# Kernel tuning notes

Hardware: AMD Instinct MI355X
Metric: run time of the kernel (lower is better)

Reference implementation:

```python
import jax, jax.numpy as jnp
import numpy as np

N_NODES = 100000
N_EDGES = 1600000
HIDDEN = 64
IN_CH = 6  # 3 (direction) + 3 (node feature part)
BN_EPS = 1e-5


def setup_inputs() -> dict:
    key = jax.random.key(0)
    ks = jax.random.split(key, 16)
    inp = {
        "x": jax.random.normal(ks[0], (N_NODES, 3), dtype=jnp.float32),
        "pos": jax.random.normal(ks[1], (N_NODES, 3), dtype=jnp.float32),
        "edge_index": jax.random.randint(ks[2], (2, N_EDGES), 0, N_NODES, dtype=jnp.int64),
    }
    dims = [IN_CH, HIDDEN, HIDDEN, HIDDEN]
    for i in range(3):
        din, dout = dims[i], dims[i + 1]
        inp[f"W{i+1}"] = jax.random.normal(ks[3 + 4 * i], (din, dout), dtype=jnp.float32) * (1.0 / np.sqrt(din))
        inp[f"b{i+1}"] = jnp.zeros((dout,), dtype=jnp.float32)
        inp[f"g{i+1}"] = jnp.ones((dout,), dtype=jnp.float32)   # BN gamma
        inp[f"be{i+1}"] = jnp.zeros((dout,), dtype=jnp.float32)  # BN beta
    return inp


def _mlp_layer(h, W, b, g, be):
    # Linear -> ReLU -> BatchNorm1d (training mode, biased variance like torch)
    h = jax.nn.relu(h @ W + b)
    mu = jnp.mean(h, axis=0)
    var = jnp.mean((h - mu) ** 2, axis=0)
    return g * (h - mu) * jax.lax.rsqrt(var + BN_EPS) + be


def reference(x, pos, edge_index, W1, b1, g1, be1, W2, b2, g2, be2, W3, b3, g3, be3):
    n = x.shape[0]
    xp = jnp.concatenate([pos, x], axis=1)             # [N, 3+F]
    src, dst = edge_index[0], edge_index[1]            # j = src, i = dst (PyG source_to_target)
    x_j = xp[src]                                      # [E, 3+F]
    x_i = xp[dst]
    direction = x_j[:, :3] - x_i[:, :3]                # [E, 3]
    # NOTE: source uses torch.norm with no dim => single global scalar norm
    direction = direction / jnp.linalg.norm(direction)
    h = jnp.concatenate([direction, x_i[:, 3:]], axis=-1)  # [E, IN_CH]
    h = _mlp_layer(h, W1, b1, g1, be1)
    h = _mlp_layer(h, W2, b2, g2, be2)
    h = _mlp_layer(h, W3, b3, g3, be3)                 # [E, HIDDEN]
    out = jax.ops.segment_max(h, dst, num_segments=n)  # scatter-max aggregation
    out = jnp.where(jnp.isfinite(out), out, 0.0)       # PyG fills empty segments with 0
    return out
```

## Files before the change

### kernel.cpp

```cpp
#include <hip/hip_runtime.h>
#include <stdint.h>

typedef unsigned short u16;
typedef unsigned int u32;
typedef __attribute__((ext_vector_type(8))) short short8;
typedef __attribute__((ext_vector_type(4))) float floatx4;

#define BN_EPS 1e-5f
#define NPB 256
#define NBMAX 512

__device__ __forceinline__ float bf2f(u16 u) { return __uint_as_float(((unsigned)u) << 16); }
__device__ __forceinline__ u16 f2bf(float f) {
  unsigned u = __float_as_uint(f);
  u += 0x7FFFu + ((u >> 16) & 1u);
  return (u16)(u >> 16);
}

__global__ void k_init(float* __restrict__ stats, u32* __restrict__ bucketTotal) {
  for (int i = threadIdx.x; i < 1024; i += blockDim.x) stats[i] = 0.f;
  for (int i = threadIdx.x; i < NBMAX + 1; i += blockDim.x) bucketTotal[i] = 0u;
}

__global__ void k_norm_hist(const int* __restrict__ ei, const float* __restrict__ pos,
                            int E, int NB, float* __restrict__ stats,
                            u32* __restrict__ bucketTotal) {
  __shared__ u32 lh[NBMAX];
  __shared__ float red[16];
  for (int i = threadIdx.x; i < NB; i += blockDim.x) lh[i] = 0u;
  __syncthreads();
  int tid = blockIdx.x * blockDim.x + threadIdx.x;
  int stride = gridDim.x * blockDim.x;
  float acc = 0.f;
  for (int e = tid; e < E; e += stride) {
    int s = ei[e], d = ei[E + e];
    float d0 = pos[3 * s + 0] - pos[3 * d + 0];
    float d1 = pos[3 * s + 1] - pos[3 * d + 1];
    float d2 = pos[3 * s + 2] - pos[3 * d + 2];
    acc = fmaf(d0, d0, acc);
    acc = fmaf(d1, d1, acc);
    acc = fmaf(d2, d2, acc);
    atomicAdd(&lh[d >> 8], 1u);
  }
#pragma unroll
  for (int off = 32; off > 0; off >>= 1) acc += __shfl_down(acc, off, 64);
  if ((threadIdx.x & 63) == 0) red[threadIdx.x >> 6] = acc;
  __syncthreads();
  if (threadIdx.x == 0) {
    float s = 0.f;
    for (int w = 0; w < (int)(blockDim.x >> 6); w++) s += red[w];
    atomicAdd(&stats[0], s);
  }
  for (int i = threadIdx.x; i < NB; i += blockDim.x)
    if (lh[i]) atomicAdd(&bucketTotal[i], lh[i]);
}

__global__ void k_scan(const u32* __restrict__ bucketTotal, u32* __restrict__ base,
                       u32* __restrict__ cursor, int NB) {
  if (threadIdx.x == 0 && blockIdx.x == 0) {
    u32 run = 0;
    for (int b = 0; b < NB; b++) {
      base[b] = run;
      cursor[b] = run;
      run += bucketTotal[b];
    }
    base[NB] = run;
  }
}

__global__ void k_place(const int* __restrict__ ei, int E, int NB,
                        u32* __restrict__ cursor, u32* __restrict__ sorted) {
  __shared__ u32 lh[NBMAX];
  __shared__ u32 lbase[NBMAX];
  for (int i = threadIdx.x; i < NB; i += blockDim.x) lh[i] = 0u;
  __syncthreads();
  int tid = blockIdx.x * blockDim.x + threadIdx.x;
  int stride = gridDim.x * blockDim.x;
  for (int e = tid; e < E; e += stride) atomicAdd(&lh[ei[E + e] >> 8], 1u);
  __syncthreads();
  for (int i = threadIdx.x; i < NB; i += blockDim.x) {
    u32 c = lh[i];
    lbase[i] = c ? atomicAdd(&cursor[i], c) : 0u;
    lh[i] = 0u;
  }
  __syncthreads();
  for (int e = tid; e < E; e += stride) {
    int d = ei[E + e];
    int b = d >> 8;
    u32 slot = lbase[b] + atomicAdd(&lh[b], 1u);
    sorted[slot] = ((u32)e << 8) | (u32)(d & 255);
  }
}

__global__ __launch_bounds__(256) void k_bucket_sort(
    const u32* __restrict__ sp, const u32* __restrict__ bbase,
    u32* __restrict__ sorted2, u32* __restrict__ nodeBase) {
  __shared__ u32 hist[NPB];
  __shared__ u32 sbase[NPB];
  int b = blockIdx.x;
  u32 start = bbase[b];
  int cnt = (int)(bbase[b + 1] - start);
  int t = threadIdx.x;
  hist[t] = 0u;
  __syncthreads();
  for (int i = t; i < cnt; i += 256) atomicAdd(&hist[sp[start + i] & 255u], 1u);
  __syncthreads();
  u32 hv = hist[t];
  sbase[t] = hv;
  __syncthreads();
  for (int off = 1; off < 256; off <<= 1) {
    u32 xx = (t >= off) ? sbase[t - off] : 0u;
    __syncthreads();
    sbase[t] += xx;
    __syncthreads();
  }
  u32 excl = sbase[t] - hv;
  __syncthreads();
  sbase[t] = start + excl;
  nodeBase[b * NPB + t] = start + excl;
  hist[t] = 0u;
  __syncthreads();
  for (int i = t; i < cnt; i += 256) {
    u32 pk = sp[start + i];
    u32 ln = pk & 255u;
    u32 slot = sbase[ln] + atomicAdd(&hist[ln], 1u);
    sorted2[slot] = pk >> 8;
  }
}

__global__ __launch_bounds__(256) void k_node_max(
    const u32* __restrict__ sorted2, const u32* __restrict__ nodeBase,
    const u16* __restrict__ h, const float* __restrict__ sc3,
    const float* __restrict__ sh3, float* __restrict__ outf, int N) {
  int lane = threadIdx.x & 63;
  int w = ((int)blockIdx.x * (blockDim.x >> 6)) + (threadIdx.x >> 6);
  int nw = (int)gridDim.x * (blockDim.x >> 6);
  float sc = sc3[lane], sh = sh3[lane];
  for (int n = w; n < N; n += nw) {
    u32 s0 = nodeBase[n];
    int cnt = (int)(nodeBase[n + 1] - s0);
    float v = -3.4e38f;
    for (int i0 = 0; i0 < cnt; i0 += 64) {
      int lim = cnt - i0;
      if (lim > 64) lim = 64;
      u32 myid = (lane < lim) ? sorted2[s0 + i0 + lane] : 0u;
#pragma unroll 4
      for (int i = 0; i < lim; i++) {
        u32 e = __shfl(myid, i, 64);
        float hf = bf2f(h[(long)e * 64 + lane]);
        v = fmaxf(v, fmaf(hf, sc, sh));
      }
    }
    outf[(long)n * 64 + lane] = (cnt == 0) ? 0.f : v;
  }
}

__global__ __launch_bounds__(256) void k_layer1(
    const int* __restrict__ ei, const float* __restrict__ pos,
    const float* __restrict__ x, const float* __restrict__ W1,
    const float* __restrict__ b1, u16* __restrict__ h,
    const float* __restrict__ stats, float* __restrict__ gsum,
    float* __restrict__ gsq, int E) {
  __shared__ float in6[6][256];
  __shared__ float ssum[64], ssq[64];
  float invn = 1.0f / sqrtf(stats[0]);
  int t = threadIdx.x;
  int lane = t & 63;
  int wv = t >> 6;
  float w[6];
#pragma unroll
  for (int k = 0; k < 6; k++) w[k] = W1[k * 64 + lane];
  float bias = b1[lane];
  float psum = 0.f, psq = 0.f;

  int chunks = (E + 255) >> 8;
  for (int c = blockIdx.x; c < chunks; c += gridDim.x) {
    long e0 = (long)c << 8;
    int e = (int)e0 + t;
    float v[6] = {0.f, 0.f, 0.f, 0.f, 0.f, 0.f};
    if (e < E) {
      int s = ei[e], d = ei[E + e];
      float p0 = pos[3 * s + 0], p1 = pos[3 * s + 1], p2 = pos[3 * s + 2];
      float q0 = pos[3 * d + 0], q1 = pos[3 * d + 1], q2 = pos[3 * d + 2];
      v[0] = (p0 - q0) * invn;
      v[1] = (p1 - q1) * invn;
      v[2] = (p2 - q2) * invn;
      v[3] = x[3 * d + 0];
      v[4] = x[3 * d + 1];
      v[5] = x[3 * d + 2];
    }
    __syncthreads();
#pragma unroll
    for (int k = 0; k < 6; k++) in6[k][t] = v[k];
    __syncthreads();
    int lim = E - (int)e0;
    if (lim > 256) lim = 256;
    int base = wv * 64;
#pragma unroll 4
    for (int i = 0; i < 64; i++) {
      int el = base + i;
      if (el >= lim) break;
      float acc = bias;
#pragma unroll
      for (int k = 0; k < 6; k++) acc = fmaf(in6[k][el], w[k], acc);
      acc = fmaxf(acc, 0.f);
      u16 hb = f2bf(acc);
      h[(e0 + el) * 64 + lane] = hb;
      float hf = bf2f(hb);
      psum += hf;
      psq = fmaf(hf, hf, psq);
    }
  }
  if (t < 64) { ssum[t] = 0.f; ssq[t] = 0.f; }
  __syncthreads();
  atomicAdd(&ssum[lane], psum);
  atomicAdd(&ssq[lane], psq);
  __syncthreads();
  if (t < 64) {
    atomicAdd(&gsum[t], ssum[t]);
    atomicAdd(&gsq[t], ssq[t]);
  }
}

__global__ void k_fin(const float* __restrict__ gsum, const float* __restrict__ gsq,
                      const float* __restrict__ g, const float* __restrict__ be,
                      float* __restrict__ scale, float* __restrict__ shift, float invE) {
  int c = threadIdx.x;
  float mu = gsum[c] * invE;
  float var = gsq[c] * invE - mu * mu;
  float s = g[c] * rsqrtf(var + BN_EPS);
  scale[c] = s;
  shift[c] = be[c] - mu * s;
}

__global__ __launch_bounds__(256) void k_layer_mfma(
    u16* h, const float* __restrict__ W, const float* __restrict__ b,
    const float* __restrict__ scale_in, const float* __restrict__ shift_in,
    float* __restrict__ gsum, float* __restrict__ gsq, int E) {
  int lane = threadIdx.x & 63;
  int m = lane & 15;
  int q = lane >> 4;

  short8 bf[4][2];
  float bias[4];
#pragma unroll
  for (int t = 0; t < 4; t++) {
    int n = t * 16 + m;
    float bb = b[n];
    for (int k = 0; k < 64; k++) bb = fmaf(shift_in[k], W[k * 64 + n], bb);
    bias[t] = bb;
#pragma unroll
    for (int s = 0; s < 2; s++)
#pragma unroll
      for (int j = 0; j < 8; j++) {
        int k = s * 32 + q * 8 + j;
        bf[t][s][j] = (short)f2bf(W[k * 64 + n] * scale_in[k]);
      }
  }

  float psum[4] = {0.f, 0.f, 0.f, 0.f}, psq[4] = {0.f, 0.f, 0.f, 0.f};

  int tiles = E >> 4;
  int gw = ((int)blockIdx.x * (blockDim.x >> 6)) + (threadIdx.x >> 6);
  int nw = (int)gridDim.x * (blockDim.x >> 6);

  for (int tile = gw; tile < tiles; tile += nw) {
    long e0 = (long)tile * 16;
    const u16* rowp = h + (e0 + m) * 64 + q * 8;
    short8 a0 = *(const short8*)(rowp);
    short8 a1 = *(const short8*)(rowp + 32);
    floatx4 acc[4];
#pragma unroll
    for (int t = 0; t < 4; t++) acc[t] = (floatx4){0.f, 0.f, 0.f, 0.f};
#pragma unroll
    for (int t = 0; t < 4; t++)
      acc[t] = __builtin_amdgcn_mfma_f32_16x16x32_bf16(a0, bf[t][0], acc[t], 0, 0, 0);
#pragma unroll
    for (int t = 0; t < 4; t++)
      acc[t] = __builtin_amdgcn_mfma_f32_16x16x32_bf16(a1, bf[t][1], acc[t], 0, 0, 0);

#pragma unroll
    for (int t = 0; t < 4; t++) {
#pragma unroll
      for (int r = 0; r < 4; r++) {
        float v = acc[t][r] + bias[t];
        v = fmaxf(v, 0.f);
        u16 hb = f2bf(v);
        h[(e0 + q * 4 + r) * 64 + t * 16 + m] = hb;
        float hf = bf2f(hb);
        psum[t] += hf;
        psq[t] = fmaf(hf, hf, psq[t]);
      }
    }
  }

#pragma unroll
  for (int t = 0; t < 4; t++) {
    psum[t] += __shfl_xor(psum[t], 16, 64);
    psum[t] += __shfl_xor(psum[t], 32, 64);
    psq[t] += __shfl_xor(psq[t], 16, 64);
    psq[t] += __shfl_xor(psq[t], 32, 64);
  }
  __shared__ float ssum[64], ssq[64];
  if (threadIdx.x < 64) { ssum[threadIdx.x] = 0.f; ssq[threadIdx.x] = 0.f; }
  __syncthreads();
  if (q == 0) {
#pragma unroll
    for (int t = 0; t < 4; t++) {
      atomicAdd(&ssum[t * 16 + m], psum[t]);
      atomicAdd(&ssq[t * 16 + m], psq[t]);
    }
  }
  __syncthreads();
  if (threadIdx.x < 64) {
    atomicAdd(&gsum[threadIdx.x], ssum[threadIdx.x]);
    atomicAdd(&gsq[threadIdx.x], ssq[threadIdx.x]);
  }
}

__global__ void k_initout(float* __restrict__ outf, long n, float* __restrict__ stats,
                          u32* __restrict__ bucketTotal) {
  long i = (long)blockIdx.x * blockDim.x + threadIdx.x;
  long stride = (long)gridDim.x * blockDim.x;
  for (long j = i; j < n; j += stride) outf[j] = __uint_as_float(0xFF800000u);
  if (i < 1024) stats[i] = 0.f;
  if (i < NBMAX + 1) bucketTotal[i] = 0u;
}
__global__ void k_scatter(const int* __restrict__ ei, const u16* __restrict__ h,
                          const float* __restrict__ scale, const float* __restrict__ shift,
                          float* outf, int E) {
  int lane = threadIdx.x & 63;
  int gw = ((int)blockIdx.x * (blockDim.x >> 6)) + (threadIdx.x >> 6);
  int nw = (int)gridDim.x * (blockDim.x >> 6);
  float sc = scale[lane], sh = shift[lane];
  for (int e = gw; e < E; e += nw) {
    int d = ei[E + e];
    float v = fmaf(bf2f(h[(long)e * 64 + lane]), sc, sh);
    float* addr = outf + (long)d * 64 + lane;
    if (v >= 0.f)
      atomicMax((int*)addr, __float_as_int(v));
    else
      atomicMin((unsigned int*)addr, __float_as_uint(v));
  }
}
__global__ void k_out(float* __restrict__ outf, long n) {
  long i = (long)blockIdx.x * blockDim.x + threadIdx.x;
  long stride = (long)gridDim.x * blockDim.x;
  for (long j = i; j < n; j += stride) {
    float v = outf[j];
    unsigned u = __float_as_uint(v);
    if ((u & 0x7F800000u) == 0x7F800000u) v = 0.f;
    outf[j] = v;
  }
}

extern "C" void kernel_launch(void* const* d_in, const int* in_sizes, int n_in,
                              void* d_out, int out_size, void* d_ws, size_t ws_size,
                              hipStream_t stream) {
  const float* x = (const float*)d_in[0];
  const float* pos = (const float*)d_in[1];
  const int* ei = (const int*)d_in[2];
  const float* W1 = (const float*)d_in[3];
  const float* b1 = (const float*)d_in[4];
  const float* g1 = (const float*)d_in[5];
  const float* be1 = (const float*)d_in[6];
  const float* W2 = (const float*)d_in[7];
  const float* b2 = (const float*)d_in[8];
  const float* g2 = (const float*)d_in[9];
  const float* be2 = (const float*)d_in[10];
  const float* W3 = (const float*)d_in[11];
  const float* b3 = (const float*)d_in[12];
  const float* g3 = (const float*)d_in[13];
  const float* be3 = (const float*)d_in[14];

  int N = in_sizes[0] / 3;
  int E = in_sizes[2] / 2;
  int NB = (N + NPB - 1) / NPB;
  long n_out = (long)N * 64;

  char* wsb = (char*)d_ws;
  u16* h = (u16*)wsb;
  size_t off = (size_t)E * 64 * 2;
  float* stats = (float*)(wsb + off);
  off += 1024 * 4;
  u32* bucketTotal = (u32*)(wsb + off);
  off += (NBMAX + 1) * 4;
  u32* baseArr = (u32*)(wsb + off);
  off += (NBMAX + 1) * 4;
  u32* cursor = (u32*)(wsb + off);
  off += NBMAX * 4;
  u32* sortedPk = (u32*)(wsb + off);
  off += (size_t)E * 4;
  u32* sorted2 = (u32*)(wsb + off);
  off += (size_t)E * 4;
  u32* nodeBase = (u32*)(wsb + off);
  off += ((size_t)NBMAX * NPB + 1) * 4;
  size_t need = off;

  float* gsum1 = stats + 64, * gsq1 = stats + 128;
  float* gsum2 = stats + 192, * gsq2 = stats + 256;
  float* gsum3 = stats + 320, * gsq3 = stats + 384;
  float* sc1 = stats + 512, * sh1 = stats + 576;
  float* sc2 = stats + 640, * sh2 = stats + 704;
  float* sc3 = stats + 768, * sh3 = stats + 832;

  float* outf = (float*)d_out;
  float invE = 1.0f / (float)E;
  bool binned = (ws_size >= need) && (NB <= NBMAX);

  if (binned) {
    k_init<<<1, 1024, 0, stream>>>(stats, bucketTotal);
    k_norm_hist<<<256, 256, 0, stream>>>(ei, pos, E, NB, stats, bucketTotal);
    k_scan<<<1, 64, 0, stream>>>(bucketTotal, baseArr, cursor, NB);
    k_place<<<256, 256, 0, stream>>>(ei, E, NB, cursor, sortedPk);
    k_bucket_sort<<<NB, 256, 0, stream>>>(sortedPk, baseArr, sorted2, nodeBase);
    k_layer1<<<1024, 256, 0, stream>>>(ei, pos, x, W1, b1, h, stats, gsum1, gsq1, E);
    k_fin<<<1, 64, 0, stream>>>(gsum1, gsq1, g1, be1, sc1, sh1, invE);
    k_layer_mfma<<<1024, 256, 0, stream>>>(h, W2, b2, sc1, sh1, gsum2, gsq2, E);
    k_fin<<<1, 64, 0, stream>>>(gsum2, gsq2, g2, be2, sc2, sh2, invE);
    k_layer_mfma<<<1024, 256, 0, stream>>>(h, W3, b3, sc2, sh2, gsum3, gsq3, E);
    k_fin<<<1, 64, 0, stream>>>(gsum3, gsq3, g3, be3, sc3, sh3, invE);
    k_node_max<<<1024, 256, 0, stream>>>(sorted2, nodeBase, h, sc3, sh3, outf, N);
  } else {
    k_initout<<<4096, 256, 0, stream>>>(outf, n_out, stats, bucketTotal);
    k_norm_hist<<<256, 256, 0, stream>>>(ei, pos, E, NB <= NBMAX ? NB : 1, stats, bucketTotal);
    k_layer1<<<1024, 256, 0, stream>>>(ei, pos, x, W1, b1, h, stats, gsum1, gsq1, E);
    k_fin<<<1, 64, 0, stream>>>(gsum1, gsq1, g1, be1, sc1, sh1, invE);
    k_layer_mfma<<<1024, 256, 0, stream>>>(h, W2, b2, sc1, sh1, gsum2, gsq2, E);
    k_fin<<<1, 64, 0, stream>>>(gsum2, gsq2, g2, be2, sc2, sh2, invE);
    k_layer_mfma<<<1024, 256, 0, stream>>>(h, W3, b3, sc2, sh2, gsum3, gsq3, E);
    k_fin<<<1, 64, 0, stream>>>(gsum3, gsq3, g3, be3, sc3, sh3, invE);
    k_scatter<<<2048, 256, 0, stream>>>(ei, h, sc3, sh3, outf, E);
    k_out<<<2048, 256, 0, stream>>>(outf, n_out);
  }
}
```

Baseline: 591.3 us.

## Compute edges in dst-sorted order so node max reads contiguous rows

Layer 1 now processes edges through the sorted permutation, so h is stored in destination-sorted order. The final per-node max then streams contiguous rows without indirection. It tracks both max and min of the raw bf16 values and applies the BN affine afterwards, picking max or min by the sign of the scale. The sentinel entry of nodeBase is written in the scan kernel, and grid sizes for several kernels are doubled. Layer 1 gathers become more random, but the scattered gather in the max kernel goes away.

```diff
diff --git a/kernel.cpp b/kernel.cpp
--- a/kernel.cpp
+++ b/kernel.cpp
@@ -56,7 +56,7 @@
 }
 
 __global__ void k_scan(const u32* __restrict__ bucketTotal, u32* __restrict__ base,
-                       u32* __restrict__ cursor, int NB) {
+                       u32* __restrict__ cursor, u32* __restrict__ nodeBase, int NB) {
   if (threadIdx.x == 0 && blockIdx.x == 0) {
     u32 run = 0;
     for (int b = 0; b < NB; b++) {
@@ -65,6 +65,7 @@
       run += bucketTotal[b];
     }
     base[NB] = run;
+    nodeBase[(size_t)NB * NPB] = run;
   }
 }
 
@@ -129,9 +130,9 @@
 }
 
 __global__ __launch_bounds__(256) void k_node_max(
-    const u32* __restrict__ sorted2, const u32* __restrict__ nodeBase,
-    const u16* __restrict__ h, const float* __restrict__ sc3,
-    const float* __restrict__ sh3, float* __restrict__ outf, int N) {
+    const u32* __restrict__ nodeBase, const u16* __restrict__ h,
+    const float* __restrict__ sc3, const float* __restrict__ sh3,
+    float* __restrict__ outf, int N) {
   int lane = threadIdx.x & 63;
   int w = ((int)blockIdx.x * (blockDim.x >> 6)) + (threadIdx.x >> 6);
   int nw = (int)gridDim.x * (blockDim.x >> 6);
@@ -139,18 +140,23 @@
   for (int n = w; n < N; n += nw) {
     u32 s0 = nodeBase[n];
     int cnt = (int)(nodeBase[n + 1] - s0);
-    float v = -3.4e38f;
-    for (int i0 = 0; i0 < cnt; i0 += 64) {
-      int lim = cnt - i0;
-      if (lim > 64) lim = 64;
-      u32 myid = (lane < lim) ? sorted2[s0 + i0 + lane] : 0u;
-#pragma unroll 4
-      for (int i = 0; i < lim; i++) {
-        u32 e = __shfl(myid, i, 64);
-        float hf = bf2f(h[(long)e * 64 + lane]);
-        v = fmaxf(v, fmaf(hf, sc, sh));
-      }
-    }
+    const u16* p = h + (long)s0 * 64 + lane;
+    float vmax = -3.4e38f, vmin = 3.4e38f;
+    int i = 0;
+    for (; i + 4 <= cnt; i += 4) {
+      float a0 = bf2f(p[(long)(i + 0) * 64]);
+      float a1 = bf2f(p[(long)(i + 1) * 64]);
+      float a2 = bf2f(p[(long)(i + 2) * 64]);
+      float a3 = bf2f(p[(long)(i + 3) * 64]);
+      vmax = fmaxf(vmax, fmaxf(fmaxf(a0, a1), fmaxf(a2, a3)));
+      vmin = fminf(vmin, fminf(fminf(a0, a1), fminf(a2, a3)));
+    }
+    for (; i < cnt; i++) {
+      float a = bf2f(p[(long)i * 64]);
+      vmax = fmaxf(vmax, a);
+      vmin = fminf(vmin, a);
+    }
+    float v = (sc >= 0.f) ? fmaf(vmax, sc, sh) : fmaf(vmin, sc, sh);
     outf[(long)n * 64 + lane] = (cnt == 0) ? 0.f : v;
   }
 }
@@ -160,7 +166,7 @@
     const float* __restrict__ x, const float* __restrict__ W1,
     const float* __restrict__ b1, u16* __restrict__ h,
     const float* __restrict__ stats, float* __restrict__ gsum,
-    float* __restrict__ gsq, int E) {
+    float* __restrict__ gsq, const u32* __restrict__ order, int E) {
   __shared__ float in6[6][256];
   __shared__ float ssum[64], ssq[64];
   float invn = 1.0f / sqrtf(stats[0]);
@@ -176,9 +182,10 @@
   int chunks = (E + 255) >> 8;
   for (int c = blockIdx.x; c < chunks; c += gridDim.x) {
     long e0 = (long)c << 8;
-    int e = (int)e0 + t;
+    int i = (int)e0 + t;
     float v[6] = {0.f, 0.f, 0.f, 0.f, 0.f, 0.f};
-    if (e < E) {
+    if (i < E) {
+      int e = order ? (int)order[i] : i;
       int s = ei[e], d = ei[E + e];
       float p0 = pos[3 * s + 0], p1 = pos[3 * s + 1], p2 = pos[3 * s + 2];
       float q0 = pos[3 * d + 0], q1 = pos[3 * d + 1], q2 = pos[3 * d + 2];
@@ -197,8 +204,8 @@
     if (lim > 256) lim = 256;
     int base = wv * 64;
 #pragma unroll 4
-    for (int i = 0; i < 64; i++) {
-      int el = base + i;
+    for (int i2 = 0; i2 < 64; i2++) {
+      int el = base + i2;
       if (el >= lim) break;
       float acc = bias;
 #pragma unroll
@@ -410,25 +417,25 @@
 
   if (binned) {
     k_init<<<1, 1024, 0, stream>>>(stats, bucketTotal);
-    k_norm_hist<<<256, 256, 0, stream>>>(ei, pos, E, NB, stats, bucketTotal);
-    k_scan<<<1, 64, 0, stream>>>(bucketTotal, baseArr, cursor, NB);
+    k_norm_hist<<<512, 256, 0, stream>>>(ei, pos, E, NB, stats, bucketTotal);
+    k_scan<<<1, 64, 0, stream>>>(bucketTotal, baseArr, cursor, nodeBase, NB);
     k_place<<<256, 256, 0, stream>>>(ei, E, NB, cursor, sortedPk);
     k_bucket_sort<<<NB, 256, 0, stream>>>(sortedPk, baseArr, sorted2, nodeBase);
-    k_layer1<<<1024, 256, 0, stream>>>(ei, pos, x, W1, b1, h, stats, gsum1, gsq1, E);
+    k_layer1<<<2048, 256, 0, stream>>>(ei, pos, x, W1, b1, h, stats, gsum1, gsq1, sorted2, E);
     k_fin<<<1, 64, 0, stream>>>(gsum1, gsq1, g1, be1, sc1, sh1, invE);
-    k_layer_mfma<<<1024, 256, 0, stream>>>(h, W2, b2, sc1, sh1, gsum2, gsq2, E);
+    k_layer_mfma<<<2048, 256, 0, stream>>>(h, W2, b2, sc1, sh1, gsum2, gsq2, E);
     k_fin<<<1, 64, 0, stream>>>(gsum2, gsq2, g2, be2, sc2, sh2, invE);
-    k_layer_mfma<<<1024, 256, 0, stream>>>(h, W3, b3, sc2, sh2, gsum3, gsq3, E);
+    k_layer_mfma<<<2048, 256, 0, stream>>>(h, W3, b3, sc2, sh2, gsum3, gsq3, E);
     k_fin<<<1, 64, 0, stream>>>(gsum3, gsq3, g3, be3, sc3, sh3, invE);
-    k_node_max<<<1024, 256, 0, stream>>>(sorted2, nodeBase, h, sc3, sh3, outf, N);
+    k_node_max<<<2048, 256, 0, stream>>>(nodeBase, h, sc3, sh3, outf, N);
   } else {
     k_initout<<<4096, 256, 0, stream>>>(outf, n_out, stats, bucketTotal);
-    k_norm_hist<<<256, 256, 0, stream>>>(ei, pos, E, NB <= NBMAX ? NB : 1, stats, bucketTotal);
-    k_layer1<<<1024, 256, 0, stream>>>(ei, pos, x, W1, b1, h, stats, gsum1, gsq1, E);
+    k_norm_hist<<<512, 256, 0, stream>>>(ei, pos, E, NB <= NBMAX ? NB : 1, stats, bucketTotal);
+    k_layer1<<<2048, 256, 0, stream>>>(ei, pos, x, W1, b1, h, stats, gsum1, gsq1, nullptr, E);
     k_fin<<<1, 64, 0, stream>>>(gsum1, gsq1, g1, be1, sc1, sh1, invE);
-    k_layer_mfma<<<1024, 256, 0, stream>>>(h, W2, b2, sc1, sh1, gsum2, gsq2, E);
+    k_layer_mfma<<<2048, 256, 0, stream>>>(h, W2, b2, sc1, sh1, gsum2, gsq2, E);
     k_fin<<<1, 64, 0, stream>>>(gsum2, gsq2, g2, be2, sc2, sh2, invE);
-    k_layer_mfma<<<1024, 256, 0, stream>>>(h, W3, b3, sc2, sh2, gsum3, gsq3, E);
+    k_layer_mfma<<<2048, 256, 0, stream>>>(h, W3, b3, sc2, sh2, gsum3, gsq3, E);
     k_fin<<<1, 64, 0, stream>>>(gsum3, gsq3, g3, be3, sc3, sh3, invE);
     k_scatter<<<2048, 256, 0, stream>>>(ei, h, sc3, sh3, outf, E);
     k_out<<<2048, 256, 0, stream>>>(outf, n_out);
```

After: 537.8 us. 1.1x faster.
